# Kernel optimization log

Measured on AMD Instinct MI355X. Metric: run time of the kernel, lower is better.

The kernel has to match this reference:

```python
import jax, jax.numpy as jnp
import numpy as np

B, S, D, H = 4, 2048, 1024, 16
HD = D // H  # head dim = 64


def setup_inputs() -> dict:
    key = jax.random.key(0)
    ks = jax.random.split(key, 11)
    scale = 1.0 / np.sqrt(D)
    return {
        "q": jax.random.normal(ks[0], (B, S, D), jnp.float32),
        "k": jax.random.normal(ks[1], (B, S, D), jnp.float32),
        "v": jax.random.normal(ks[2], (B, S, D), jnp.float32),
        "w_q": jax.random.normal(ks[3], (D, D), jnp.float32) * scale,
        "b_q": jax.random.normal(ks[4], (D,), jnp.float32) * scale,
        "w_k": jax.random.normal(ks[5], (D, D), jnp.float32) * scale,
        "b_k": jax.random.normal(ks[6], (D,), jnp.float32) * scale,
        "w_v": jax.random.normal(ks[7], (D, D), jnp.float32) * scale,
        "b_v": jax.random.normal(ks[8], (D,), jnp.float32) * scale,
        "w_o": jax.random.normal(ks[9], (D, D), jnp.float32) * scale,
        "b_o": jax.random.normal(ks[10], (D,), jnp.float32) * scale,
    }


def _split_heads(x):
    # [B,S,D] -> [B,H,S,HD]
    return x.reshape(B, S, H, HD).transpose(0, 2, 1, 3)


def reference(q, k, v, w_q, b_q, w_k, b_k, w_v, b_v, w_o, b_o):
    qh = _split_heads(q @ w_q + b_q)
    kh = _split_heads(k @ w_k + b_k)
    vh = _split_heads(v @ w_v + b_v)
    # full score matrix [B,H,S,S], as in the naive torch code
    score = jnp.einsum("bhqd,bhkd->bhqk", qh, kh) / jnp.sqrt(jnp.float32(HD))
    attn = jax.nn.softmax(score, axis=-1)
    out = jnp.einsum("bhqk,bhkd->bhqd", attn, vh)
    out = out.transpose(0, 2, 1, 3).reshape(B, S, D)
    return out @ w_o + b_o
```

## Files before the change

kernel.cpp:

```cpp
#include <hip/hip_runtime.h>
#include <hip/hip_bf16.h>

#define BB 4
#define SS 2048
#define DD 1024
#define HH 16
#define HDD 64
#define MM (BB*SS)

using bf16x8 = __attribute__((ext_vector_type(8))) short;
using f32x4  = __attribute__((ext_vector_type(4))) float;
using f32x16 = __attribute__((ext_vector_type(16))) float;

static __device__ __forceinline__ ushort f2bf(float f) {
    __hip_bfloat16 h = __float2bfloat16(f);
    return *reinterpret_cast<ushort*>(&h);
}

static __device__ __forceinline__ void gload_lds16(const ushort* g, ushort* l) {
    __builtin_amdgcn_global_load_lds(
        (const __attribute__((address_space(1))) unsigned int*)g,
        (__attribute__((address_space(3))) unsigned int*)l, 16, 0, 0);
}

static __device__ __forceinline__ unsigned cvtpk(float lo, float hi) {
    unsigned r;
    asm("v_cvt_pk_bf16_f32 %0, %1, %2" : "=v"(r) : "v"(lo), "v"(hi));
    return r;
}

static __device__ __forceinline__ float exp2_raw(float x) {
    float r;
    asm("v_exp_f32 %0, %1" : "=v"(r) : "v"(x));
    return r;
}

static __device__ __forceinline__ void halfswap(unsigned& a, unsigned& b, int hi) {
#if __has_builtin(__builtin_amdgcn_permlane32_swap)
    typedef int v2i __attribute__((ext_vector_type(2)));
    v2i r = __builtin_amdgcn_permlane32_swap((int)a, (int)b, false, false);
    a = (unsigned)r.x; b = (unsigned)r.y;
#else
    unsigned xa = (unsigned)__shfl_xor((int)a, 32);
    unsigned xb = (unsigned)__shfl_xor((int)b, 32);
    unsigned na = hi ? xb : a;
    unsigned nb = hi ? b : xa;
    a = na; b = nb;
#endif
}

#define PIPE_BAR(N) do {                                          \
    asm volatile("s_waitcnt vmcnt(" #N ")" ::: "memory");         \
    __builtin_amdgcn_sched_barrier(0);                            \
    __builtin_amdgcn_s_barrier();                                 \
    __builtin_amdgcn_sched_barrier(0);                            \
} while (0)

__global__ __launch_bounds__(256) void cast3_bf16_k(
    const float* __restrict__ q, const float* __restrict__ k,
    const float* __restrict__ v, ushort* __restrict__ qo,
    ushort* __restrict__ ko, ushort* __restrict__ vo)
{
    const float* in; ushort* out;
    switch (blockIdx.y) {
        case 0:  in = q; out = qo; break;
        case 1:  in = k; out = ko; break;
        default: in = v; out = vo; break;
    }
    const size_t i = ((size_t)blockIdx.x * 256 + threadIdx.x) * 8;
    float4 a = *(const float4*)(in + i);
    float4 b = *(const float4*)(in + i + 4);
    short r[8];
    r[0] = (short)f2bf(a.x); r[1] = (short)f2bf(a.y);
    r[2] = (short)f2bf(a.z); r[3] = (short)f2bf(a.w);
    r[4] = (short)f2bf(b.x); r[5] = (short)f2bf(b.y);
    r[6] = (short)f2bf(b.z); r[7] = (short)f2bf(b.w);
    *(bf16x8*)(out + i) = *(const bf16x8*)r;
}

__global__ __launch_bounds__(256) void wtrans_k(
    const float* __restrict__ w0, const float* __restrict__ w1,
    const float* __restrict__ w2, const float* __restrict__ w3,
    ushort* __restrict__ o0, ushort* __restrict__ o1,
    ushort* __restrict__ o2, ushort* __restrict__ o3)
{
    __shared__ float tile[32][33];
    const float* W; ushort* O;
    switch (blockIdx.z) {
        case 0:  W = w0; O = o0; break;
        case 1:  W = w1; O = o1; break;
        case 2:  W = w2; O = o2; break;
        default: W = w3; O = o3; break;
    }
    const int tx = threadIdx.x & 31, ty = threadIdx.x >> 5;
    const int n0 = blockIdx.x * 32, k0 = blockIdx.y * 32;
    #pragma unroll
    for (int i = 0; i < 4; i++)
        tile[ty * 4 + i][tx] = W[(size_t)(k0 + ty * 4 + i) * DD + n0 + tx];
    __syncthreads();
    #pragma unroll
    for (int i = 0; i < 4; i++)
        O[(size_t)(n0 + ty * 4 + i) * DD + k0 + tx] = f2bf(tile[tx][ty * 4 + i]);
}

template<int MODE>
__global__ __launch_bounds__(256) void gemm_mfma_k(
    const ushort* __restrict__ A, const ushort* __restrict__ WT,
    const float* __restrict__ bias, void* __restrict__ Cout)
{
    __shared__ ushort As[128 * 32];
    __shared__ ushort Bs[128 * 32];

    const int t  = threadIdx.x;
    const int w  = t >> 6;
    const int l  = t & 63;
    const int lr = l & 15;
    const int lg = l >> 4;
    const int wr = w >> 1, wc = w & 1;

    int bid = blockIdx.x;
    bid = (bid & 7) * 64 + (bid >> 3);
    const int mt = bid >> 3, nt = bid & 7;
    const int m0 = mt * 128, n0 = nt * 128;

    const int srow = l >> 2;
    const int scol = (l & 3) * 8;

    f32x4 acc[4][4];
    #pragma unroll
    for (int mi = 0; mi < 4; mi++)
        #pragma unroll
        for (int ni = 0; ni < 4; ni++)
            acc[mi][ni] = (f32x4){0.f, 0.f, 0.f, 0.f};

    const ushort* Ab = A  + (size_t)m0 * DD;
    const ushort* Bb = WT + (size_t)n0 * DD;

    for (int k0 = 0; k0 < DD; k0 += 32) {
        __syncthreads();
        #pragma unroll
        for (int j = 0; j < 2; j++) {
            const int rbase = (w * 2 + j) * 16;
            gload_lds16(Ab + (size_t)(rbase + srow) * DD + k0 + scol, &As[rbase * 32]);
            gload_lds16(Bb + (size_t)(rbase + srow) * DD + k0 + scol, &Bs[rbase * 32]);
        }
        __syncthreads();

        bf16x8 af[4], bfr[4];
        #pragma unroll
        for (int mi = 0; mi < 4; mi++)
            af[mi] = *(const bf16x8*)&As[(wr * 64 + mi * 16 + lr) * 32 + lg * 8];
        #pragma unroll
        for (int ni = 0; ni < 4; ni++)
            bfr[ni] = *(const bf16x8*)&Bs[(wc * 64 + ni * 16 + lr) * 32 + lg * 8];
        #pragma unroll
        for (int mi = 0; mi < 4; mi++)
            #pragma unroll
            for (int ni = 0; ni < 4; ni++)
                acc[mi][ni] = __builtin_amdgcn_mfma_f32_16x16x32_bf16(
                    af[mi], bfr[ni], acc[mi][ni], 0, 0, 0);
    }

    #pragma unroll
    for (int mi = 0; mi < 4; mi++) {
        #pragma unroll
        for (int ni = 0; ni < 4; ni++) {
            const int c  = n0 + wc * 64 + ni * 16 + lr;
            const float bc = bias[c];
            const int r0 = m0 + wr * 64 + mi * 16 + lg * 4;
            if (MODE == 0) {
                float* Co = (float*)Cout;
                #pragma unroll
                for (int rg = 0; rg < 4; rg++)
                    Co[(size_t)(r0 + rg) * DD + c] = acc[mi][ni][rg] + bc;
            } else if (MODE == 3) {
                const int bi = r0 >> 11, si = r0 & 2047;
                const int hi = c >> 6,  hd = c & 63;
                ushort pk[4];
                #pragma unroll
                for (int rg = 0; rg < 4; rg++)
                    pk[rg] = f2bf(acc[mi][ni][rg] + bc);
                ushort* O = (ushort*)Cout;
                *(uint2*)&O[(((size_t)(bi * HH + hi) * HDD) + hd) * SS + si] =
                    *(const uint2*)pk;
            } else {
                const float sc = (MODE == 2) ? 0.180336880111f : 1.0f;
                ushort* O = (ushort*)Cout;
                #pragma unroll
                for (int rg = 0; rg < 4; rg++) {
                    const int r = r0 + rg;
                    const int bi = r >> 11, si = r & 2047;
                    const int hi = c >> 6,  hd = c & 63;
                    O[(((size_t)(bi * HH + hi) * SS) + si) * HDD + hd] =
                        f2bf((acc[mi][ni][rg] + bc) * sc);
                }
            }
        }
    }
}

__global__ __launch_bounds__(256, 2) void flash_attn_mfma(
    const ushort* __restrict__ qh, const ushort* __restrict__ kh,
    const ushort* __restrict__ vt, ushort* __restrict__ ctx)
{
    __shared__ ushort smem[16384];

    const int t  = threadIdx.x;
    const int w  = t >> 6;
    const int l  = t & 63;
    const int hi = l >> 5;
    const int lq = l & 31;

    const int wg = (blockIdx.x & 7) * 64 + (blockIdx.x >> 3);
    const int bi = wg >> 7;
    const int h  = (wg >> 3) & 15;
    const int q0 = (wg & 7) * 256;

    const size_t base  = (size_t)(bi * HH + h) * SS * HDD;
    const size_t basev = (size_t)(bi * HH + h) * HDD * SS;

    bf16x8 qf0[4], qf1[4];
    {
        const ushort* qp0 = qh + base + (size_t)(q0 + w * 64 + lq) * HDD;
        const ushort* qp1 = qp0 + 32 * HDD;
        #pragma unroll
        for (int ds = 0; ds < 4; ds++) {
            qf0[ds] = *(const bf16x8*)(qp0 + ds * 16 + hi * 8);
            qf1[ds] = *(const bf16x8*)(qp1 + ds * 16 + hi * 8);
        }
    }

    f32x16 o00 = {}, o01 = {}, o10 = {}, o11 = {};
    float l0 = 0.f, l1 = 0.f;

    const int rsub = l >> 3;
    const int csw  = ((l & 7) ^ rsub) * 8;
    auto stageK = [&](int buf, int kv) {
        #pragma unroll
        for (int j = 0; j < 2; j++) {
            const int rb = 16 * w + 8 * j;
            gload_lds16(kh + base + (size_t)(kv + rb + rsub) * HDD + csw,
                        &smem[buf * 4096 + rb * 64]);
        }
    };
    auto stageV = [&](int buf, int kv) {
        #pragma unroll
        for (int j = 0; j < 2; j++) {
            const int rb = 16 * w + 8 * j;
            gload_lds16(vt + basev + (size_t)(rb + rsub) * SS + kv + csw,
                        &smem[8192 + buf * 4096 + rb * 64]);
        }
    };

    auto qk2 = [&](const ushort* KB, int kvh, f32x16& sg0, f32x16& sg1) {
        sg0 = (f32x16){};
        sg1 = (f32x16){};
        __builtin_amdgcn_s_setprio(1);
        #pragma unroll
        for (int ds = 0; ds < 4; ds++) {
            const int slot = ((ds * 2 + hi) ^ (l & 7)) * 8;
            bf16x8 ka = *(const bf16x8*)&KB[(kvh * 32 + lq) * 64 + slot];
            sg0 = __builtin_amdgcn_mfma_f32_32x32x16_bf16(ka, qf0[ds], sg0, 0, 0, 0);
            sg1 = __builtin_amdgcn_mfma_f32_32x32x16_bf16(ka, qf1[ds], sg1, 0, 0, 0);
        }
        __builtin_amdgcn_s_setprio(0);
    };

    auto finish16 = [&](f32x16& s, float& lacc, bf16x8* pa2) {
        float t0 = 0.f, t1 = 0.f, t2 = 0.f, t3 = 0.f;
        #pragma unroll
        for (int r = 0; r < 16; r += 4) {
            s[r + 0] = exp2_raw(s[r + 0]); t0 += s[r + 0];
            s[r + 1] = exp2_raw(s[r + 1]); t1 += s[r + 1];
            s[r + 2] = exp2_raw(s[r + 2]); t2 += s[r + 2];
            s[r + 3] = exp2_raw(s[r + 3]); t3 += s[r + 3];
        }
        lacc += (t0 + t1) + (t2 + t3);
        #pragma unroll
        for (int sblk = 0; sblk < 2; sblk++) {
            const int ob = sblk * 8;
            unsigned a = cvtpk(s[ob + 0], s[ob + 1]);
            unsigned b = cvtpk(s[ob + 4], s[ob + 5]);
            halfswap(a, b, hi);
            unsigned c = cvtpk(s[ob + 2], s[ob + 3]);
            unsigned d = cvtpk(s[ob + 6], s[ob + 7]);
            halfswap(c, d, hi);
            union { unsigned u[4]; bf16x8 v; } fr;
            fr.u[0] = a; fr.u[1] = c; fr.u[2] = b; fr.u[3] = d;
            pa2[sblk] = fr.v;
        }
    };

    auto pvhalf = [&](const ushort* VB, int kvh,
                      const bf16x8* pg0, const bf16x8* pg1) {
        __builtin_amdgcn_s_setprio(1);
        #pragma unroll
        for (int ksl = 0; ksl < 2; ksl++) {
            const int ks = kvh * 2 + ksl;
            const int slot = ((ks * 2 + hi) ^ (l & 7)) * 8;
            bf16x8 vb0 = *(const bf16x8*)&VB[lq * 64 + slot];
            bf16x8 vb1 = *(const bf16x8*)&VB[(32 + lq) * 64 + slot];
            o00 = __builtin_amdgcn_mfma_f32_32x32x16_bf16(pg0[ksl], vb0, o00, 0, 0, 0);
            o01 = __builtin_amdgcn_mfma_f32_32x32x16_bf16(pg0[ksl], vb1, o01, 0, 0, 0);
            o10 = __builtin_amdgcn_mfma_f32_32x32x16_bf16(pg1[ksl], vb0, o10, 0, 0, 0);
            o11 = __builtin_amdgcn_mfma_f32_32x32x16_bf16(pg1[ksl], vb1, o11, 0, 0, 0);
        }
        __builtin_amdgcn_s_setprio(0);
    };

    stageK(0, 0); stageV(0, 0);
    int cur = 0;

    for (int tt = 0; tt < 32; tt++) {
        PIPE_BAR(0);
        if (tt + 1 < 32) { stageK(cur ^ 1, (tt + 1) * 64);
                           stageV(cur ^ 1, (tt + 1) * 64); }

        const ushort* KB = &smem[cur * 4096];
        const ushort* VB = &smem[8192 + cur * 4096];

        f32x16 sA, sB, sC, sD;
        qk2(KB, 0, sA, sB);
        qk2(KB, 1, sC, sD);

        bf16x8 pg0[2], pg1[2];
        finish16(sA, l0, pg0);
        finish16(sB, l1, pg1);
        pvhalf(VB, 0, pg0, pg1);
        finish16(sC, l0, pg0);
        finish16(sD, l1, pg1);
        pvhalf(VB, 1, pg0, pg1);

        cur ^= 1;
    }

    const float ls0 = l0 + __shfl_xor(l0, 32);
    const float ls1 = l1 + __shfl_xor(l1, 32);
    const float iv0 = 1.0f / ls0;
    const float iv1 = 1.0f / ls1;
    #pragma unroll
    for (int r = 0; r < 16; r++) {
        const int qq = (r & 3) + 8 * (r >> 2) + 4 * hi;
        const float a0 = __shfl(iv0, qq);
        const float a1 = __shfl(iv1, qq);
        const int row0 = q0 + w * 64 + qq;
        ushort* op0 = ctx + (size_t)(bi * SS + row0) * DD + h * HDD;
        op0[lq]      = f2bf(o00[r] * a0);
        op0[32 + lq] = f2bf(o01[r] * a0);
        ushort* op1 = op0 + (size_t)32 * DD;
        op1[lq]      = f2bf(o10[r] * a1);
        op1[32 + lq] = f2bf(o11[r] * a1);
    }
}

extern "C" void kernel_launch(void* const* d_in, const int* in_sizes, int n_in,
                              void* d_out, int out_size, void* d_ws, size_t ws_size,
                              hipStream_t stream) {
    const float* q   = (const float*)d_in[0];
    const float* k   = (const float*)d_in[1];
    const float* v   = (const float*)d_in[2];
    const float* w_q = (const float*)d_in[3];
    const float* b_q = (const float*)d_in[4];
    const float* w_k = (const float*)d_in[5];
    const float* b_k = (const float*)d_in[6];
    const float* w_v = (const float*)d_in[7];
    const float* b_v = (const float*)d_in[8];
    const float* w_o = (const float*)d_in[9];
    const float* b_o = (const float*)d_in[10];
    float* out = (float*)d_out;

    const size_t SZ = (size_t)BB * SS * DD;
    const size_t WZ = (size_t)DD * DD;
    ushort* ws2  = (ushort*)d_ws;
    ushort* qh   = ws2;
    ushort* kh   = ws2 + SZ;
    ushort* vt   = ws2 + 2 * SZ;
    ushort* ctxb = ws2 + 3 * SZ;
    ushort* qbf  = ws2 + 4 * SZ;
    ushort* kbf  = ws2 + 5 * SZ;
    ushort* vbf  = ws2 + 6 * SZ;
    ushort* wqT  = ws2 + 7 * SZ;
    ushort* wkT  = wqT + WZ;
    ushort* wvT  = wkT + WZ;
    ushort* woT  = wvT + WZ;

    const int castBlocks = (int)(SZ / (256 * 8));
    cast3_bf16_k<<<dim3(castBlocks, 3), 256, 0, stream>>>(q, k, v, qbf, kbf, vbf);
    wtrans_k<<<dim3(32, 32, 4), 256, 0, stream>>>(w_q, w_k, w_v, w_o,
                                                  wqT, wkT, wvT, woT);

    const int gblocks = (MM / 128) * (DD / 128);
    gemm_mfma_k<2><<<gblocks, 256, 0, stream>>>(qbf, wqT, b_q, qh);
    gemm_mfma_k<1><<<gblocks, 256, 0, stream>>>(kbf, wkT, b_k, kh);
    gemm_mfma_k<3><<<gblocks, 256, 0, stream>>>(vbf, wvT, b_v, vt);

    flash_attn_mfma<<<dim3(512), 256, 0, stream>>>(qh, kh, vt, ctxb);

    gemm_mfma_k<0><<<gblocks, 256, 0, stream>>>(ctxb, woT, b_o, out);
}
```

Measured before the change: 209.9 us.

## Fuse fp32-to-bf16 input cast into a single batched QKV projection GEMM

Removes the separate cast kernel for q/k/v. The projection GEMM now loads fp32 activations into registers, converts them to bf16, and writes them into padded LDS, prefetching the next k-slice while the current one is consumed. The three projection GEMMs become one launch of 1536 blocks that select their operands by segment. This drops a full bf16 write and reread of the activations plus two launches. In exchange, the A operand is read at twice the width per GEMM tile, and the kernel uses more registers and hand-placed waitcnt and barriers.

```diff
diff --git a/kernel.cpp b/kernel.cpp
--- a/kernel.cpp
+++ b/kernel.cpp
@@ -55,28 +55,6 @@
     __builtin_amdgcn_s_barrier();                                 \
     __builtin_amdgcn_sched_barrier(0);                            \
 } while (0)
-
-__global__ __launch_bounds__(256) void cast3_bf16_k(
-    const float* __restrict__ q, const float* __restrict__ k,
-    const float* __restrict__ v, ushort* __restrict__ qo,
-    ushort* __restrict__ ko, ushort* __restrict__ vo)
-{
-    const float* in; ushort* out;
-    switch (blockIdx.y) {
-        case 0:  in = q; out = qo; break;
-        case 1:  in = k; out = ko; break;
-        default: in = v; out = vo; break;
-    }
-    const size_t i = ((size_t)blockIdx.x * 256 + threadIdx.x) * 8;
-    float4 a = *(const float4*)(in + i);
-    float4 b = *(const float4*)(in + i + 4);
-    short r[8];
-    r[0] = (short)f2bf(a.x); r[1] = (short)f2bf(a.y);
-    r[2] = (short)f2bf(a.z); r[3] = (short)f2bf(a.w);
-    r[4] = (short)f2bf(b.x); r[5] = (short)f2bf(b.y);
-    r[6] = (short)f2bf(b.z); r[7] = (short)f2bf(b.w);
-    *(bf16x8*)(out + i) = *(const bf16x8*)r;
-}
 
 __global__ __launch_bounds__(256) void wtrans_k(
     const float* __restrict__ w0, const float* __restrict__ w1,
@@ -103,13 +81,29 @@
         O[(size_t)(n0 + ty * 4 + i) * DD + k0 + tx] = f2bf(tile[tx][ty * 4 + i]);
 }
 
-template<int MODE>
-__global__ __launch_bounds__(256) void gemm_mfma_k(
-    const ushort* __restrict__ A, const ushort* __restrict__ WT,
-    const float* __restrict__ bias, void* __restrict__ Cout)
+__global__ __launch_bounds__(256) void gemm_qkv_k(
+    const float* __restrict__ qi, const float* __restrict__ ki,
+    const float* __restrict__ vi,
+    const ushort* __restrict__ wqT, const ushort* __restrict__ wkT,
+    const ushort* __restrict__ wvT,
+    const float* __restrict__ b_q, const float* __restrict__ b_k,
+    const float* __restrict__ b_v,
+    ushort* __restrict__ qo, ushort* __restrict__ ko, ushort* __restrict__ vo)
 {
-    __shared__ ushort As[128 * 32];
+    __shared__ ushort As[128 * 40];
     __shared__ ushort Bs[128 * 32];
+
+    const int seg = blockIdx.x >> 9;
+    int bid = blockIdx.x & 511;
+    bid = (bid & 7) * 64 + (bid >> 3);
+    const int mt = bid >> 3, nt = bid & 7;
+    const int m0 = mt * 128, n0 = nt * 128;
+
+    const float*  A32  = seg == 0 ? qi  : seg == 1 ? ki  : vi;
+    const ushort* WT   = seg == 0 ? wqT : seg == 1 ? wkT : wvT;
+    const float*  bias = seg == 0 ? b_q : seg == 1 ? b_k : b_v;
+    ushort*       Cout = seg == 0 ? qo  : seg == 1 ? ko  : vo;
+    const float   sc   = seg == 0 ? 0.180336880111f : 1.0f;
 
     const int t  = threadIdx.x;
     const int w  = t >> 6;
@@ -118,11 +112,8 @@
     const int lg = l >> 4;
     const int wr = w >> 1, wc = w & 1;
 
-    int bid = blockIdx.x;
-    bid = (bid & 7) * 64 + (bid >> 3);
-    const int mt = bid >> 3, nt = bid & 7;
-    const int m0 = mt * 128, n0 = nt * 128;
-
+    const int ar = t >> 2;
+    const int ac = (t & 3) * 8;
     const int srow = l >> 2;
     const int scol = (l & 3) * 8;
 
@@ -133,23 +124,53 @@
         for (int ni = 0; ni < 4; ni++)
             acc[mi][ni] = (f32x4){0.f, 0.f, 0.f, 0.f};
 
-    const ushort* Ab = A  + (size_t)m0 * DD;
-    const ushort* Bb = WT + (size_t)n0 * DD;
+    const float*  Ab = A32 + (size_t)m0 * DD;
+    const ushort* Bb = WT  + (size_t)n0 * DD;
+
+    float4 a0[2], a1[2];
+    #pragma unroll
+    for (int j = 0; j < 2; j++) {
+        const float* p = Ab + (size_t)(ar + 64 * j) * DD + ac;
+        a0[j] = *(const float4*)p;
+        a1[j] = *(const float4*)(p + 4);
+    }
 
     for (int k0 = 0; k0 < DD; k0 += 32) {
-        __syncthreads();
+        __builtin_amdgcn_s_barrier();
+        #pragma unroll
+        for (int j = 0; j < 2; j++) {
+            union { unsigned u[4]; bf16x8 v8; } fr;
+            fr.u[0] = cvtpk(a0[j].x, a0[j].y);
+            fr.u[1] = cvtpk(a0[j].z, a0[j].w);
+            fr.u[2] = cvtpk(a1[j].x, a1[j].y);
+            fr.u[3] = cvtpk(a1[j].z, a1[j].w);
+            *(bf16x8*)&As[(ar + 64 * j) * 40 + ac] = fr.v8;
+        }
         #pragma unroll
         for (int j = 0; j < 2; j++) {
             const int rbase = (w * 2 + j) * 16;
-            gload_lds16(Ab + (size_t)(rbase + srow) * DD + k0 + scol, &As[rbase * 32]);
-            gload_lds16(Bb + (size_t)(rbase + srow) * DD + k0 + scol, &Bs[rbase * 32]);
-        }
-        __syncthreads();
+            gload_lds16(Bb + (size_t)(rbase + srow) * DD + k0 + scol,
+                        &Bs[rbase * 32]);
+        }
+        __builtin_amdgcn_sched_barrier(0);
+        {
+            const int kn = (k0 + 32 < DD) ? k0 + 32 : 0;
+            #pragma unroll
+            for (int j = 0; j < 2; j++) {
+                const float* p = Ab + (size_t)(ar + 64 * j) * DD + kn + ac;
+                a0[j] = *(const float4*)p;
+                a1[j] = *(const float4*)(p + 4);
+            }
+        }
+        asm volatile("s_waitcnt vmcnt(4) lgkmcnt(0)" ::: "memory");
+        __builtin_amdgcn_sched_barrier(0);
+        __builtin_amdgcn_s_barrier();
+        __builtin_amdgcn_sched_barrier(0);
 
         bf16x8 af[4], bfr[4];
         #pragma unroll
         for (int mi = 0; mi < 4; mi++)
-            af[mi] = *(const bf16x8*)&As[(wr * 64 + mi * 16 + lr) * 32 + lg * 8];
+            af[mi] = *(const bf16x8*)&As[(wr * 64 + mi * 16 + lr) * 40 + lg * 8];
         #pragma unroll
         for (int ni = 0; ni < 4; ni++)
             bfr[ni] = *(const bf16x8*)&Bs[(wc * 64 + ni * 16 + lr) * 32 + lg * 8];
@@ -168,33 +189,96 @@
             const int c  = n0 + wc * 64 + ni * 16 + lr;
             const float bc = bias[c];
             const int r0 = m0 + wr * 64 + mi * 16 + lg * 4;
-            if (MODE == 0) {
-                float* Co = (float*)Cout;
-                #pragma unroll
-                for (int rg = 0; rg < 4; rg++)
-                    Co[(size_t)(r0 + rg) * DD + c] = acc[mi][ni][rg] + bc;
-            } else if (MODE == 3) {
+            if (seg == 2) {
                 const int bi = r0 >> 11, si = r0 & 2047;
                 const int hi = c >> 6,  hd = c & 63;
                 ushort pk[4];
                 #pragma unroll
                 for (int rg = 0; rg < 4; rg++)
                     pk[rg] = f2bf(acc[mi][ni][rg] + bc);
-                ushort* O = (ushort*)Cout;
-                *(uint2*)&O[(((size_t)(bi * HH + hi) * HDD) + hd) * SS + si] =
+                *(uint2*)&Cout[(((size_t)(bi * HH + hi) * HDD) + hd) * SS + si] =
                     *(const uint2*)pk;
             } else {
-                const float sc = (MODE == 2) ? 0.180336880111f : 1.0f;
-                ushort* O = (ushort*)Cout;
                 #pragma unroll
                 for (int rg = 0; rg < 4; rg++) {
                     const int r = r0 + rg;
                     const int bi = r >> 11, si = r & 2047;
                     const int hi = c >> 6,  hd = c & 63;
-                    O[(((size_t)(bi * HH + hi) * SS) + si) * HDD + hd] =
+                    Cout[(((size_t)(bi * HH + hi) * SS) + si) * HDD + hd] =
                         f2bf((acc[mi][ni][rg] + bc) * sc);
                 }
             }
+        }
+    }
+}
+
+__global__ __launch_bounds__(256) void gemm_out_k(
+    const ushort* __restrict__ A, const ushort* __restrict__ WT,
+    const float* __restrict__ bias, float* __restrict__ Cout)
+{
+    __shared__ ushort As[128 * 32];
+    __shared__ ushort Bs[128 * 32];
+
+    const int t  = threadIdx.x;
+    const int w  = t >> 6;
+    const int l  = t & 63;
+    const int lr = l & 15;
+    const int lg = l >> 4;
+    const int wr = w >> 1, wc = w & 1;
+
+    int bid = blockIdx.x;
+    bid = (bid & 7) * 64 + (bid >> 3);
+    const int mt = bid >> 3, nt = bid & 7;
+    const int m0 = mt * 128, n0 = nt * 128;
+
+    const int srow = l >> 2;
+    const int scol = (l & 3) * 8;
+
+    f32x4 acc[4][4];
+    #pragma unroll
+    for (int mi = 0; mi < 4; mi++)
+        #pragma unroll
+        for (int ni = 0; ni < 4; ni++)
+            acc[mi][ni] = (f32x4){0.f, 0.f, 0.f, 0.f};
+
+    const ushort* Ab = A  + (size_t)m0 * DD;
+    const ushort* Bb = WT + (size_t)n0 * DD;
+
+    for (int k0 = 0; k0 < DD; k0 += 32) {
+        __syncthreads();
+        #pragma unroll
+        for (int j = 0; j < 2; j++) {
+            const int rbase = (w * 2 + j) * 16;
+            gload_lds16(Ab + (size_t)(rbase + srow) * DD + k0 + scol, &As[rbase * 32]);
+            gload_lds16(Bb + (size_t)(rbase + srow) * DD + k0 + scol, &Bs[rbase * 32]);
+        }
+        __syncthreads();
+
+        bf16x8 af[4], bfr[4];
+        #pragma unroll
+        for (int mi = 0; mi < 4; mi++)
+            af[mi] = *(const bf16x8*)&As[(wr * 64 + mi * 16 + lr) * 32 + lg * 8];
+        #pragma unroll
+        for (int ni = 0; ni < 4; ni++)
+            bfr[ni] = *(const bf16x8*)&Bs[(wc * 64 + ni * 16 + lr) * 32 + lg * 8];
+        #pragma unroll
+        for (int mi = 0; mi < 4; mi++)
+            #pragma unroll
+            for (int ni = 0; ni < 4; ni++)
+                acc[mi][ni] = __builtin_amdgcn_mfma_f32_16x16x32_bf16(
+                    af[mi], bfr[ni], acc[mi][ni], 0, 0, 0);
+    }
+
+    #pragma unroll
+    for (int mi = 0; mi < 4; mi++) {
+        #pragma unroll
+        for (int ni = 0; ni < 4; ni++) {
+            const int c  = n0 + wc * 64 + ni * 16 + lr;
+            const float bc = bias[c];
+            const int r0 = m0 + wr * 64 + mi * 16 + lg * 4;
+            #pragma unroll
+            for (int rg = 0; rg < 4; rg++)
+                Cout[(size_t)(r0 + rg) * DD + c] = acc[mi][ni][rg] + bc;
         }
     }
 }
@@ -376,25 +460,18 @@
     ushort* kh   = ws2 + SZ;
     ushort* vt   = ws2 + 2 * SZ;
     ushort* ctxb = ws2 + 3 * SZ;
-    ushort* qbf  = ws2 + 4 * SZ;
-    ushort* kbf  = ws2 + 5 * SZ;
-    ushort* vbf  = ws2 + 6 * SZ;
-    ushort* wqT  = ws2 + 7 * SZ;
+    ushort* wqT  = ws2 + 4 * SZ;
     ushort* wkT  = wqT + WZ;
     ushort* wvT  = wkT + WZ;
     ushort* woT  = wvT + WZ;
 
-    const int castBlocks = (int)(SZ / (256 * 8));
-    cast3_bf16_k<<<dim3(castBlocks, 3), 256, 0, stream>>>(q, k, v, qbf, kbf, vbf);
     wtrans_k<<<dim3(32, 32, 4), 256, 0, stream>>>(w_q, w_k, w_v, w_o,
                                                   wqT, wkT, wvT, woT);
 
-    const int gblocks = (MM / 128) * (DD / 128);
-    gemm_mfma_k<2><<<gblocks, 256, 0, stream>>>(qbf, wqT, b_q, qh);
-    gemm_mfma_k<1><<<gblocks, 256, 0, stream>>>(kbf, wkT, b_k, kh);
-    gemm_mfma_k<3><<<gblocks, 256, 0, stream>>>(vbf, wvT, b_v, vt);
+    gemm_qkv_k<<<dim3(1536), 256, 0, stream>>>(q, k, v, wqT, wkT, wvT,
+                                               b_q, b_k, b_v, qh, kh, vt);
 
     flash_attn_mfma<<<dim3(512), 256, 0, stream>>>(qh, kh, vt, ctxb);
 
-    gemm_mfma_k<0><<<gblocks, 256, 0, stream>>>(ctxb, woT, b_o, out);
-}
+    gemm_out_k<<<dim3(512), 256, 0, stream>>>(ctxb, woT, b_o, out);
+}
```

Result: faster. 182.7 us, median of 2 (-12.9%).
